# Performance work log

Hardware: AMD Instinct MI355X
Metric: run time of the kernel (lower is better)

## Reference

```python
import jax, jax.numpy as jnp
import numpy as np

N, P, C, H, W = 2, 100, 256, 128, 192
K = 3; KK = K * K; E = C * KK; NH = 8; DH = E // NH; FFN = 2048


def _ln(x, g, b, eps=1e-5):
    m = x.mean(-1, keepdims=True)
    v = ((x - m) ** 2).mean(-1, keepdims=True)
    return (x - m) * jax.lax.rsqrt(v + eps) * g + b


def setup_inputs():
    ks = iter(jax.random.split(jax.random.key(0), 64))
    def rnd(shape, s=1.0):
        return jax.random.normal(next(ks), shape, jnp.float32) * s
    z = lambda *s: jnp.zeros(s, jnp.float32)
    o = lambda *s: jnp.ones(s, jnp.float32)
    return {
        'x': rnd((N, C, H, W)),
        'proposal_feat': rnd((N, P, E)),
        'mask_preds': rnd((N, P, H, W)),
        'ku_dyn_w': rnd((2 * C, C), 0.02), 'ku_dyn_b': z(2 * C),
        'ku_in_w': rnd((2 * C, C), 0.02), 'ku_in_b': z(2 * C),
        'ku_ig_w': rnd((C, C), 0.02), 'ku_ig_b': z(C),
        'ku_ug_w': rnd((C, C), 0.02), 'ku_ug_b': z(C),
        'ku_nin_g': o(C), 'ku_nin_b': z(C),
        'ku_nout_g': o(C), 'ku_nout_b': z(C),
        'ku_inin_g': o(C), 'ku_inin_b': z(C),
        'ku_inout_g': o(C), 'ku_inout_b': z(C),
        'ku_fc_w': rnd((C, C), 0.02), 'ku_fc_b': z(C),
        'ku_fcn_g': o(C), 'ku_fcn_b': z(C),
        'attn_in_w': rnd((3 * E, E), 0.02), 'attn_in_b': z(3 * E),
        'attn_out_w': rnd((E, E), 0.02), 'attn_out_b': z(E),
        'attn_ln_g': o(E), 'attn_ln_b': z(E),
        'ffn_w1': rnd((FFN, C), 0.02), 'ffn_b1': z(FFN),
        'ffn_w2': rnd((C, FFN), 0.02), 'ffn_b2': z(C),
        'ffn_ln_g': o(C), 'ffn_ln_b': z(C),
        'mask_fc_ws': rnd((3, C, C), 0.02),
        'mask_fc_ln_g': o(3, C), 'mask_fc_ln_b': z(3, C),
        'fc_mask_w': rnd((C, C), 0.02), 'fc_mask_b': z(C),
    }


def _forward(x, proposal_feat, mask_preds, ku_dyn_w, ku_dyn_b, ku_in_w, ku_in_b,
             ku_ig_w, ku_ig_b, ku_ug_w, ku_ug_b, ku_nin_g, ku_nin_b, ku_nout_g,
             ku_nout_b, ku_inin_g, ku_inin_b, ku_inout_g, ku_inout_b, ku_fc_w,
             ku_fc_b, ku_fcn_g, ku_fcn_b, attn_in_w, attn_in_b, attn_out_w,
             attn_out_b, attn_ln_g, attn_ln_b, ffn_w1, ffn_b1, ffn_w2, ffn_b2,
             ffn_ln_g, ffn_ln_b, mask_fc_ws, mask_fc_ln_g, mask_fc_ln_b,
             fc_mask_w, fc_mask_b):
    # mask-softmax pooling over proposals: (N,P,H,W) x (N,C,H,W) -> (N,P,C)
    sig = jax.nn.softmax(mask_preds, axis=1)
    x_feat = jnp.einsum('bnhw,bchw->bnc', sig, x)

    # KernelUpdator (gated dynamic kernel update)
    pf = proposal_feat.reshape(N, P, C, KK).transpose(0, 1, 3, 2).reshape(N * P, KK, C)
    upd = x_feat.reshape(N * P, C)
    params = upd @ ku_dyn_w.T + ku_dyn_b            # (NP, 2C)
    p_in, p_out = params[:, :C], params[:, C:]
    inp = pf @ ku_in_w.T + ku_in_b                  # (NP, KK, 2C)
    i_in, i_out = inp[..., :C], inp[..., C:]
    gate = i_in * p_in[:, None, :]                  # (NP, KK, C)
    ig = jax.nn.sigmoid(_ln(gate @ ku_ig_w.T + ku_ig_b, ku_inin_g, ku_inin_b))
    ug = jax.nn.sigmoid(_ln(gate @ ku_ug_w.T + ku_ug_b, ku_nin_g, ku_nin_b))
    p_out = _ln(p_out, ku_nout_g, ku_nout_b)
    i_out = _ln(i_out, ku_inout_g, ku_inout_b)
    feat = ug * p_out[:, None, :] + ig * i_out
    feat = jax.nn.relu(_ln(feat @ ku_fc_w.T + ku_fc_b, ku_fcn_g, ku_fcn_b))  # (NP,KK,C)

    # self-attention across proposals; embed dim E = C*K*K, with residual + LN
    obj = feat.reshape(N, P, E).transpose(1, 0, 2)  # (P,N,E)
    qkv = obj @ attn_in_w.T + attn_in_b
    q, k, v = jnp.split(qkv, 3, axis=-1)
    q = q.reshape(P, N, NH, DH) * np.float32(1.0 / np.sqrt(DH))
    k = k.reshape(P, N, NH, DH)
    v = v.reshape(P, N, NH, DH)
    a = jax.nn.softmax(jnp.einsum('qnhd,knhd->nhqk', q, k), axis=-1)
    o = jnp.einsum('nhqk,knhd->qnhd', a, v).reshape(P, N, E)
    obj = _ln(obj + o @ attn_out_w.T + attn_out_b, attn_ln_g, attn_ln_b)
    obj = obj.transpose(1, 0, 2).reshape(N, P, KK, C)

    # FFN (residual) + LN, applied per (proposal, kernel position)
    h = jax.nn.relu(obj @ ffn_w1.T + ffn_b1) @ ffn_w2.T + ffn_b2
    obj = _ln(obj + h, ffn_ln_g, ffn_ln_b)

    mf = obj
    for i in range(3):
        mf = jax.nn.relu(_ln(mf @ mask_fc_ws[i].T, mask_fc_ln_g[i], mask_fc_ln_b[i]))
    mf = mf @ fc_mask_w.T + fc_mask_b               # (N,P,KK,C)
    kernels = mf.transpose(0, 1, 3, 2).reshape(N, P, C, K, K)

    # per-image dynamic conv: vmap replaces the python loop over batch
    def conv_one(xi, wi):
        return jax.lax.conv_general_dilated(
            xi[None], wi, (1, 1), 'SAME',
            dimension_numbers=('NCHW', 'OIHW', 'NCHW'))[0]
    new_masks = jax.vmap(conv_one)(x, kernels)      # (N,P,H,W)

    obj_kernels = obj.transpose(0, 1, 3, 2).reshape(N, P, C, K, K)
    return new_masks, obj_kernels


def reference(x, proposal_feat, mask_preds, ku_dyn_w, ku_dyn_b, ku_in_w, ku_in_b,
              ku_ig_w, ku_ig_b, ku_ug_w, ku_ug_b, ku_nin_g, ku_nin_b, ku_nout_g,
              ku_nout_b, ku_inin_g, ku_inin_b, ku_inout_g, ku_inout_b, ku_fc_w,
              ku_fc_b, ku_fcn_g, ku_fcn_b, attn_in_w, attn_in_b, attn_out_w,
              attn_out_b, attn_ln_g, attn_ln_b, ffn_w1, ffn_b1, ffn_w2, ffn_b2,
              ffn_ln_g, ffn_ln_b, mask_fc_ws, mask_fc_ln_g, mask_fc_ln_b,
              fc_mask_w, fc_mask_b):
    return _forward(x, proposal_feat, mask_preds, ku_dyn_w, ku_dyn_b, ku_in_w,
                    ku_in_b, ku_ig_w, ku_ig_b, ku_ug_w, ku_ug_b, ku_nin_g,
                    ku_nin_b, ku_nout_g, ku_nout_b, ku_inin_g, ku_inin_b,
                    ku_inout_g, ku_inout_b, ku_fc_w, ku_fc_b, ku_fcn_g, ku_fcn_b,
                    attn_in_w, attn_in_b, attn_out_w, attn_out_b, attn_ln_g,
                    attn_ln_b, ffn_w1, ffn_b1, ffn_w2, ffn_b2, ffn_ln_g,
                    ffn_ln_b, mask_fc_ws, mask_fc_ln_g, mask_fc_ln_b,
                    fc_mask_w, fc_mask_b)
```

## Files before the change

kernel.cpp:

```cpp
#include <hip/hip_runtime.h>
#include <hip/hip_bf16.h>

#define N_ 2
#define P_ 100
#define C_ 256
#define H_ 128
#define W_ 192
#define HW_ 24576
#define KK_ 9
#define E_ 2304
#define NH_ 8
#define DH_ 288
#define FFN_ 2048
#define NP_ 200
#define ROWS_ 1800
#define XKC_ 64

typedef __attribute__((ext_vector_type(8))) __bf16 bf16x8;
typedef __attribute__((ext_vector_type(4))) float f32x4;

__global__ __launch_bounds__(256) void k_softmax(const float* __restrict__ mp, float* __restrict__ sig){
  int idx = blockIdx.x*256 + threadIdx.x;
  if(idx >= N_*HW_) return;
  int n = idx / HW_, hw = idx - n*HW_;
  const float* base = mp + (size_t)n*P_*HW_ + hw;
  float m = -1e30f;
  for(int p=0;p<P_;p++) m = fmaxf(m, base[(size_t)p*HW_]);
  float s = 0.f;
  for(int p=0;p<P_;p++) s += __expf(base[(size_t)p*HW_] - m);
  float inv = 1.f/s;
  float* ob = sig + (size_t)n*P_*HW_ + hw;
  for(int p=0;p<P_;p++) ob[(size_t)p*HW_] = __expf(base[(size_t)p*HW_] - m)*inv;
}

__global__ __launch_bounds__(256) void k_permute_pf(const float* __restrict__ prop, float* __restrict__ pf){
  int i = blockIdx.x*256 + threadIdx.x;
  if(i >= ROWS_*C_) return;
  int c = i & 255;
  int r = i >> 8;
  int kk = r % 9, np = r / 9;
  pf[i] = prop[(size_t)np*E_ + c*KK_ + kk];
}

__global__ __launch_bounds__(256) void k_xfeat1m(const float* __restrict__ sig, const float* __restrict__ x,
                                                 float* __restrict__ partial){
  const int ct = blockIdx.x, kb = blockIdx.y, n = blockIdx.z;
  const int hw0 = kb*384;
  const int tid = threadIdx.x;
  const int wid = tid >> 6, lane = tid & 63;
  const int col = lane & 15, quad = lane >> 4;
  const int wm = wid & 1, wn = wid >> 1;
  const int MT = wm ? 3 : 4;
  __shared__ __bf16 As[112][72];
  __shared__ __bf16 Bs[128][72];
  f32x4 acc[4][4] = {};
  for(int k0=0; k0<384; k0+=64){
    __syncthreads();
    for(int i=tid; i<896; i+=256){
      int p = i >> 3, kg = i & 7;
      bf16x8 v;
      if(p < P_){
        const float* sp = &sig[((size_t)n*P_ + p)*HW_ + hw0 + k0 + kg*8];
        const float4 f0 = *(const float4*)sp;
        const float4 f1 = *(const float4*)(sp+4);
        v[0]=(__bf16)f0.x; v[1]=(__bf16)f0.y; v[2]=(__bf16)f0.z; v[3]=(__bf16)f0.w;
        v[4]=(__bf16)f1.x; v[5]=(__bf16)f1.y; v[6]=(__bf16)f1.z; v[7]=(__bf16)f1.w;
      } else {
        #pragma unroll
        for(int u=0;u<8;u++) v[u] = (__bf16)0.f;
      }
      *(bf16x8*)&As[p][kg*8] = v;
    }
    for(int i=tid; i<1024; i+=256){
      int c = i >> 3, kg = i & 7;
      const float* xp = &x[((size_t)n*C_ + ct*128 + c)*HW_ + hw0 + k0 + kg*8];
      const float4 f0 = *(const float4*)xp;
      const float4 f1 = *(const float4*)(xp+4);
      bf16x8 v;
      v[0]=(__bf16)f0.x; v[1]=(__bf16)f0.y; v[2]=(__bf16)f0.z; v[3]=(__bf16)f0.w;
      v[4]=(__bf16)f1.x; v[5]=(__bf16)f1.y; v[6]=(__bf16)f1.z; v[7]=(__bf16)f1.w;
      *(bf16x8*)&Bs[c][kg*8] = v;
    }
    __syncthreads();
    #pragma unroll
    for(int ks=0; ks<2; ks++){
      bf16x8 b[4];
      #pragma unroll
      for(int t=0;t<4;t++) b[t] = *(const bf16x8*)&Bs[(wn*4+t)*16 + col][ks*32 + quad*8];
      #pragma unroll
      for(int mt=0; mt<4; mt++){
        if(mt < MT){
          bf16x8 a = *(const bf16x8*)&As[(wm*4+mt)*16 + col][ks*32 + quad*8];
          #pragma unroll
          for(int t=0;t<4;t++)
            acc[mt][t] = __builtin_amdgcn_mfma_f32_16x16x32_bf16(a, b[t], acc[mt][t], 0, 0, 0);
        }
      }
    }
  }
  #pragma unroll
  for(int mt=0; mt<4; mt++){
    if(mt < MT){
      #pragma unroll
      for(int r=0;r<4;r++){
        int p = (wm*4+mt)*16 + quad*4 + r;
        if(p < P_){
          float* op = &partial[(((size_t)n*XKC_ + kb)*P_ + p)*C_ + ct*128 + wn*64 + col];
          #pragma unroll
          for(int t=0;t<4;t++) op[t*16] = acc[mt][t][r];
        }
      }
    }
  }
}

__global__ __launch_bounds__(256) void k_xfeat2(const float* __restrict__ partial, float* __restrict__ xfeat){
  int np = blockIdx.x;
  int n = np / P_, p = np - n*P_;
  int c = threadIdx.x;
  float s = 0.f;
  for(int kb=0;kb<XKC_;kb++) s += partial[(((size_t)n*XKC_ + kb)*P_ + p)*C_ + c];
  xfeat[(size_t)np*C_ + c] = s;
}

__global__ __launch_bounds__(256) void k_gemm_mfma(const float* __restrict__ A, const float* __restrict__ Wt,
    const float* __restrict__ bias, float* __restrict__ out, int M, int N, int K, int act)
{
  const int n0 = blockIdx.x*128, m0 = blockIdx.y*64;
  const int tid = threadIdx.x;
  const int wid = tid >> 6, lane = tid & 63;
  const int col = lane & 15, quad = lane >> 4;
  const int wm = wid & 1, wn = wid >> 1;
  __shared__ __bf16 As[64][72];
  __shared__ __bf16 Bs[128][72];
  f32x4 acc[2][4] = {};
  for(int k0=0; k0<K; k0+=64){
    __syncthreads();
    for(int i=tid; i<512; i+=256){
      int r = i >> 3, kg = i & 7;
      int m = m0 + r;
      bf16x8 v;
      if(m < M){
        const float* ap = &A[(size_t)m*K + k0 + kg*8];
        const float4 f0 = *(const float4*)ap;
        const float4 f1 = *(const float4*)(ap+4);
        v[0]=(__bf16)f0.x; v[1]=(__bf16)f0.y; v[2]=(__bf16)f0.z; v[3]=(__bf16)f0.w;
        v[4]=(__bf16)f1.x; v[5]=(__bf16)f1.y; v[6]=(__bf16)f1.z; v[7]=(__bf16)f1.w;
      } else {
        #pragma unroll
        for(int u=0;u<8;u++) v[u] = (__bf16)0.f;
      }
      *(bf16x8*)&As[r][kg*8] = v;
    }
    for(int i=tid; i<1024; i+=256){
      int r = i >> 3, kg = i & 7;
      const float* wp = &Wt[(size_t)(n0 + r)*K + k0 + kg*8];
      const float4 f0 = *(const float4*)wp;
      const float4 f1 = *(const float4*)(wp+4);
      bf16x8 v;
      v[0]=(__bf16)f0.x; v[1]=(__bf16)f0.y; v[2]=(__bf16)f0.z; v[3]=(__bf16)f0.w;
      v[4]=(__bf16)f1.x; v[5]=(__bf16)f1.y; v[6]=(__bf16)f1.z; v[7]=(__bf16)f1.w;
      *(bf16x8*)&Bs[r][kg*8] = v;
    }
    __syncthreads();
    #pragma unroll
    for(int ks=0; ks<2; ks++){
      bf16x8 b[4], a[2];
      #pragma unroll
      for(int t=0;t<4;t++) b[t] = *(const bf16x8*)&Bs[(wn*4+t)*16 + col][ks*32 + quad*8];
      #pragma unroll
      for(int mt=0;mt<2;mt++) a[mt] = *(const bf16x8*)&As[(wm*2+mt)*16 + col][ks*32 + quad*8];
      #pragma unroll
      for(int mt=0;mt<2;mt++)
        #pragma unroll
        for(int t=0;t<4;t++)
          acc[mt][t] = __builtin_amdgcn_mfma_f32_16x16x32_bf16(a[mt], b[t], acc[mt][t], 0, 0, 0);
    }
  }
  #pragma unroll
  for(int mt=0;mt<2;mt++){
    #pragma unroll
    for(int r=0;r<4;r++){
      int m = m0 + (wm*2+mt)*16 + quad*4 + r;
      if(m < M){
        #pragma unroll
        for(int t=0;t<4;t++){
          int n = n0 + (wn*4+t)*16 + col;
          float v = acc[mt][t][r];
          if(bias) v += bias[n];
          if(act == 1) v = fmaxf(v, 0.f);
          out[(size_t)m*N + n] = v;
        }
      }
    }
  }
}

__global__ __launch_bounds__(256) void k_gemm_splitk(const float* __restrict__ A, const float* __restrict__ Wt,
    float* __restrict__ part, int M, int N, int K, int KC)
{
  const int n0 = blockIdx.x*128, m0 = blockIdx.y*64;
  const int kz = blockIdx.z*KC;
  const int tid = threadIdx.x;
  const int wid = tid >> 6, lane = tid & 63;
  const int col = lane & 15, quad = lane >> 4;
  const int wm = wid & 1, wn = wid >> 1;
  __shared__ __bf16 As[64][72];
  __shared__ __bf16 Bs[128][72];
  f32x4 acc[2][4] = {};
  for(int k0=kz; k0<kz+KC; k0+=64){
    __syncthreads();
    for(int i=tid; i<512; i+=256){
      int r = i >> 3, kg = i & 7;
      int m = m0 + r;
      bf16x8 v;
      if(m < M){
        const float* ap = &A[(size_t)m*K + k0 + kg*8];
        const float4 f0 = *(const float4*)ap;
        const float4 f1 = *(const float4*)(ap+4);
        v[0]=(__bf16)f0.x; v[1]=(__bf16)f0.y; v[2]=(__bf16)f0.z; v[3]=(__bf16)f0.w;
        v[4]=(__bf16)f1.x; v[5]=(__bf16)f1.y; v[6]=(__bf16)f1.z; v[7]=(__bf16)f1.w;
      } else {
        #pragma unroll
        for(int u=0;u<8;u++) v[u] = (__bf16)0.f;
      }
      *(bf16x8*)&As[r][kg*8] = v;
    }
    for(int i=tid; i<1024; i+=256){
      int r = i >> 3, kg = i & 7;
      const float* wp = &Wt[(size_t)(n0 + r)*K + k0 + kg*8];
      const float4 f0 = *(const float4*)wp;
      const float4 f1 = *(const float4*)(wp+4);
      bf16x8 v;
      v[0]=(__bf16)f0.x; v[1]=(__bf16)f0.y; v[2]=(__bf16)f0.z; v[3]=(__bf16)f0.w;
      v[4]=(__bf16)f1.x; v[5]=(__bf16)f1.y; v[6]=(__bf16)f1.z; v[7]=(__bf16)f1.w;
      *(bf16x8*)&Bs[r][kg*8] = v;
    }
    __syncthreads();
    #pragma unroll
    for(int ks=0; ks<2; ks++){
      bf16x8 b[4], a[2];
      #pragma unroll
      for(int t=0;t<4;t++) b[t] = *(const bf16x8*)&Bs[(wn*4+t)*16 + col][ks*32 + quad*8];
      #pragma unroll
      for(int mt=0;mt<2;mt++) a[mt] = *(const bf16x8*)&As[(wm*2+mt)*16 + col][ks*32 + quad*8];
      #pragma unroll
      for(int mt=0;mt<2;mt++)
        #pragma unroll
        for(int t=0;t<4;t++)
          acc[mt][t] = __builtin_amdgcn_mfma_f32_16x16x32_bf16(a[mt], b[t], acc[mt][t], 0, 0, 0);
    }
  }
  float* pbase = part + (size_t)blockIdx.z*M*N;
  #pragma unroll
  for(int mt=0;mt<2;mt++){
    #pragma unroll
    for(int r=0;r<4;r++){
      int m = m0 + (wm*2+mt)*16 + quad*4 + r;
      if(m < M){
        #pragma unroll
        for(int t=0;t<4;t++){
          int n = n0 + (wn*4+t)*16 + col;
          pbase[(size_t)m*N + n] = acc[mt][t][r];
        }
      }
    }
  }
}

__global__ __launch_bounds__(256) void k_redk(const float* __restrict__ part, const float* __restrict__ bias,
    float* __restrict__ out, int M, int N, int S)
{
  size_t i4 = ((size_t)blockIdx.x*256 + threadIdx.x)*4;
  size_t MN = (size_t)M*N;
  if(i4 >= MN) return;
  float4 s = *(const float4*)&part[i4];
  for(int z=1; z<S; z++){
    const float4 p = *(const float4*)&part[(size_t)z*MN + i4];
    s.x+=p.x; s.y+=p.y; s.z+=p.z; s.w+=p.w;
  }
  if(bias){
    int n = (int)(i4 % (size_t)N);
    const float4 b = *(const float4*)&bias[n];
    s.x+=b.x; s.y+=b.y; s.z+=b.z; s.w+=b.w;
  }
  *(float4*)&out[i4] = s;
}

__global__ __launch_bounds__(256) void k_ln256(const float* __restrict__ in, const float* __restrict__ res,
    const float* __restrict__ g, const float* __restrict__ b, float* __restrict__ out, int M, int act)
{
  int row = blockIdx.x*4 + (threadIdx.x >> 6);
  int lane = threadIdx.x & 63;
  if(row >= M) return;
  float4 v = *(const float4*)&in[(size_t)row*C_ + lane*4];
  if(res){
    const float4 rv = *(const float4*)&res[(size_t)row*C_ + lane*4];
    v.x += rv.x; v.y += rv.y; v.z += rv.z; v.w += rv.w;
  }
  float s = v.x + v.y + v.z + v.w;
  float q = v.x*v.x + v.y*v.y + v.z*v.z + v.w*v.w;
  #pragma unroll
  for(int off=32; off; off>>=1){ s += __shfl_xor(s, off, 64); q += __shfl_xor(q, off, 64); }
  float mean = s*(1.f/256.f);
  float rstd = rsqrtf(q*(1.f/256.f) - mean*mean + 1e-5f);
  const float4 gv = *(const float4*)&g[lane*4];
  const float4 bv = *(const float4*)&b[lane*4];
  float o[4] = {(v.x-mean)*rstd*gv.x + bv.x, (v.y-mean)*rstd*gv.y + bv.y,
                (v.z-mean)*rstd*gv.z + bv.z, (v.w-mean)*rstd*gv.w + bv.w};
  #pragma unroll
  for(int j=0;j<4;j++){
    if(act==1) o[j] = fmaxf(o[j], 0.f);
    else if(act==2) o[j] = 1.f/(1.f + __expf(-o[j]));
  }
  float4 ov = {o[0],o[1],o[2],o[3]};
  *(float4*)&out[(size_t)row*C_ + lane*4] = ov;
}

__global__ __launch_bounds__(256) void k_gate(const float* __restrict__ inp, const float* __restrict__ params,
                                              float* __restrict__ gate){
  int i = blockIdx.x*256 + threadIdx.x;
  if(i >= ROWS_*C_) return;
  int c = i & 255, r = i >> 8;
  int np = r / 9;
  gate[i] = inp[(size_t)r*512 + c] * params[(size_t)np*512 + c];
}

__device__ __forceinline__ void block_stats(float v, float* red, int slot, float& mean, float& rstd){
  float s = v, q = v*v;
  #pragma unroll
  for(int off=32; off; off>>=1){ s += __shfl_xor(s, off, 64); q += __shfl_xor(q, off, 64); }
  int wid = threadIdx.x >> 6;
  if((threadIdx.x & 63) == 0){ red[slot + wid] = s; red[slot + 4 + wid] = q; }
  __syncthreads();
  s = red[slot+0]+red[slot+1]+red[slot+2]+red[slot+3];
  q = red[slot+4]+red[slot+5]+red[slot+6]+red[slot+7];
  mean = s*(1.f/256.f);
  rstd = rsqrtf(q*(1.f/256.f) - mean*mean + 1e-5f);
}

__global__ __launch_bounds__(256) void k_combine(const float* __restrict__ params, const float* __restrict__ inp,
  const float* __restrict__ ug, const float* __restrict__ ig,
  const float* __restrict__ nout_g, const float* __restrict__ nout_b,
  const float* __restrict__ inout_g, const float* __restrict__ inout_b,
  float* __restrict__ feat)
{
  __shared__ float red[16];
  int r = blockIdx.x;
  int np = r / 9;
  int c = threadIdx.x;
  float pv = params[(size_t)np*512 + 256 + c];
  float mean, rstd;
  block_stats(pv, red, 0, mean, rstd);
  float pn = (pv - mean)*rstd*nout_g[c] + nout_b[c];
  float iv = inp[(size_t)r*512 + 256 + c];
  float mean2, rstd2;
  block_stats(iv, red, 8, mean2, rstd2);
  float iw = (iv - mean2)*rstd2*inout_g[c] + inout_b[c];
  size_t o = (size_t)r*C_ + c;
  feat[o] = ug[o]*pn + ig[o]*iw;
}

__global__ __launch_bounds__(256) void k_attn2(const float* __restrict__ qkv, float* __restrict__ attnO){
  const int qt = blockIdx.x, h = blockIdx.y, n = blockIdx.z;
  const int q0 = qt*10;
  const int tid = threadIdx.x;
  __shared__ float Qs[10][292];
  __shared__ float KVs[25][292];
  __shared__ float Ss[10][104];
  const float scale = 0.05892556509887896f;
  const size_t base = (size_t)n*P_*6912 + (size_t)h*DH_;
  for(int i=tid; i<10*DH_; i+=256){
    int qi = i/DH_, d = i - qi*DH_;
    Qs[qi][d] = qkv[base + (size_t)(q0+qi)*6912 + d] * scale;
  }
  for(int kt=0; kt<4; kt++){
    int kp0 = kt*25;
    __syncthreads();
    for(int i=tid; i<25*DH_; i+=256){
      int ki = i/DH_, d = i - ki*DH_;
      KVs[ki][d] = qkv[base + (size_t)(kp0+ki)*6912 + E_ + d];
    }
    __syncthreads();
    if(tid < 250){
      int qi = tid/25, ki = tid - qi*25;
      float s = 0.f;
      #pragma unroll 9
      for(int d=0; d<DH_; d+=4){
        const float4 a = *(const float4*)&Qs[qi][d];
        const float4 b = *(const float4*)&KVs[ki][d];
        s += a.x*b.x + a.y*b.y + a.z*b.z + a.w*b.w;
      }
      Ss[qi][kp0+ki] = s;
    }
  }
  __syncthreads();
  {
    int w = tid >> 6, lane = tid & 63;
    for(int r=w; r<10; r+=4){
      float v0 = (lane < 100) ? Ss[r][lane] : -1e30f;
      float v1 = (lane < 36)  ? Ss[r][64+lane] : -1e30f;
      float m = fmaxf(v0, v1);
      #pragma unroll
      for(int off=32; off; off>>=1) m = fmaxf(m, __shfl_xor(m, off, 64));
      float e0 = (lane < 100) ? __expf(v0-m) : 0.f;
      float e1 = (lane < 36)  ? __expf(v1-m) : 0.f;
      float s = e0 + e1;
      #pragma unroll
      for(int off=32; off; off>>=1) s += __shfl_xor(s, off, 64);
      float inv = 1.f/s;
      if(lane < 100) Ss[r][lane] = e0*inv;
      if(lane < 36)  Ss[r][64+lane] = e1*inv;
    }
  }
  float acc[12];
  #pragma unroll
  for(int j=0;j<12;j++) acc[j]=0.f;
  for(int kt=0; kt<4; kt++){
    int kp0 = kt*25;
    __syncthreads();
    for(int i=tid; i<25*DH_; i+=256){
      int ki = i/DH_, d = i - ki*DH_;
      KVs[ki][d] = qkv[base + (size_t)(kp0+ki)*6912 + 2*E_ + d];
    }
    __syncthreads();
    int j = 0;
    for(int i=tid; i<10*DH_; i+=256, j++){
      int qi = i/DH_, d = i - qi*DH_;
      float s = acc[j];
      #pragma unroll
      for(int ki=0; ki<25; ki++) s += Ss[qi][kp0+ki]*KVs[ki][d];
      acc[j] = s;
    }
  }
  {
    int j = 0;
    for(int i=tid; i<10*DH_; i+=256, j++){
      int qi = i/DH_, d = i - qi*DH_;
      attnO[(size_t)(n*P_ + q0 + qi)*E_ + h*DH_ + d] = acc[j];
    }
  }
}

__global__ __launch_bounds__(256) void k_add_ln2304(const float* __restrict__ obj0, const float* __restrict__ tp,
  const float* __restrict__ g, const float* __restrict__ b, float* __restrict__ out)
{
  __shared__ float red[8];
  int row = blockIdx.x;
  float v[9]; float s=0.f, q=0.f;
  #pragma unroll
  for(int j=0;j<9;j++){
    int e = threadIdx.x + j*256;
    float t = obj0[(size_t)row*E_ + e] + tp[(size_t)row*E_ + e];
    v[j]=t; s+=t; q+=t*t;
  }
  #pragma unroll
  for(int off=32; off; off>>=1){ s += __shfl_xor(s, off, 64); q += __shfl_xor(q, off, 64); }
  int wid = threadIdx.x>>6;
  if((threadIdx.x&63)==0){ red[wid]=s; red[4+wid]=q; }
  __syncthreads();
  s = red[0]+red[1]+red[2]+red[3]; q = red[4]+red[5]+red[6]+red[7];
  float mean = s*(1.f/2304.f);
  float rstd = rsqrtf(q*(1.f/2304.f) - mean*mean + 1e-5f);
  #pragma unroll
  for(int j=0;j<9;j++){
    int e = threadIdx.x + j*256;
    out[(size_t)row*E_ + e] = (v[j]-mean)*rstd*g[e] + b[e];
  }
}

__global__ __launch_bounds__(256) void k_objk(const float* __restrict__ obj2, float* __restrict__ outk){
  int i = blockIdx.x*256 + threadIdx.x;
  if(i >= ROWS_*C_) return;
  int kk = i % 9; int t = i / 9; int c = t & 255; int np = t >> 8;
  outk[i] = obj2[((size_t)np*9 + kk)*C_ + c];
}

__global__ __launch_bounds__(256) void k_conv_mfma(const float* __restrict__ x, const float* __restrict__ ker,
                                                   float* __restrict__ out){
  const int wt = blockIdx.x, ht = blockIdx.y, z = blockIdx.z;
  const int n = z >> 1, ps = z & 1;
  const int pbase = ps*64;
  const int NT = ps ? 3 : 4;
  const int tid = threadIdx.x;
  const int hi = tid >> 6;
  const int lane = tid & 63;
  const int col = lane & 15, quad = lane >> 4;
  const int w0 = wt*64, h0 = ht*4;

  __shared__ __bf16 xs[6][66][32];
  __shared__ __bf16 ks[9][64][32];

  f32x4 acc[4][4] = {};
  const int npr = NT*16;

  for(int c0=0; c0<C_; c0+=32){
    __syncthreads();
    for(int i=tid; i<1584; i+=256){
      int oct = i / 396;
      int rem = i - oct*396;
      int hy = rem / 66, wx = rem - hy*66;
      int hh = h0 - 1 + hy, ww = w0 - 1 + wx;
      bf16x8 v;
      if(hh >= 0 && hh < H_ && ww >= 0 && ww < W_){
        const float* xp = &x[(((size_t)n*C_ + c0 + oct*8)*H_ + hh)*W_ + ww];
        #pragma unroll
        for(int u=0;u<8;u++) v[u] = (__bf16)xp[(size_t)u*HW_];
      } else {
        #pragma unroll
        for(int u=0;u<8;u++) v[u] = (__bf16)0.f;
      }
      *(bf16x8*)&xs[hy][wx][oct*8] = v;
    }
    for(int i=tid; i<9*npr*4; i+=256){
      int oct = i & 3;
      int t = i >> 2;
      int tap = t / npr, pl = t - tap*npr;
      int p = pbase + pl;
      bf16x8 v;
      if(p < P_){
        const float* kp = &ker[((size_t)(n*P_+p)*9 + tap)*C_ + c0 + oct*8];
        #pragma unroll
        for(int u=0;u<8;u++) v[u] = (__bf16)kp[u];
      } else {
        #pragma unroll
        for(int u=0;u<8;u++) v[u] = (__bf16)0.f;
      }
      *(bf16x8*)&ks[tap][pl][oct*8] = v;
    }
    __syncthreads();
    #pragma unroll
    for(int ky=0; ky<3; ky++){
      #pragma unroll
      for(int kx=0; kx<3; kx++){
        const int tap = ky*3 + kx;
        const int hy = hi + ky;
        bf16x8 b[4];
        #pragma unroll
        for(int t=0;t<4;t++) b[t] = *(const bf16x8*)&xs[hy][t*16 + col + kx][quad*8];
        #pragma unroll
        for(int pt=0; pt<4; pt++){
          if(pt < NT){
            bf16x8 a = *(const bf16x8*)&ks[tap][pt*16 + col][quad*8];
            #pragma unroll
            for(int t=0;t<4;t++)
              acc[pt][t] = __builtin_amdgcn_mfma_f32_16x16x32_bf16(a, b[t], acc[pt][t], 0, 0, 0);
          }
        }
      }
    }
  }
  const int h = h0 + hi;
  #pragma unroll
  for(int pt=0; pt<4; pt++){
    if(pt < NT){
      #pragma unroll
      for(int r=0;r<4;r++){
        int p = pbase + pt*16 + quad*4 + r;
        if(p < P_){
          float* op = &out[((size_t)(n*P_+p)*H_ + h)*W_ + w0 + col];
          #pragma unroll
          for(int t=0;t<4;t++) op[t*16] = acc[pt][t][r];
        }
      }
    }
  }
}

extern "C" void kernel_launch(void* const* d_in, const int* in_sizes, int n_in,
                              void* d_out, int out_size, void* d_ws, size_t ws_size,
                              hipStream_t stream)
{
  (void)in_sizes; (void)n_in; (void)out_size; (void)ws_size;
  const float* x          = (const float*)d_in[0];
  const float* prop       = (const float*)d_in[1];
  const float* mask_pred  = (const float*)d_in[2];
  const float* ku_dyn_w   = (const float*)d_in[3];
  const float* ku_dyn_b   = (const float*)d_in[4];
  const float* ku_in_w    = (const float*)d_in[5];
  const float* ku_in_b    = (const float*)d_in[6];
  const float* ku_ig_w    = (const float*)d_in[7];
  const float* ku_ig_b    = (const float*)d_in[8];
  const float* ku_ug_w    = (const float*)d_in[9];
  const float* ku_ug_b    = (const float*)d_in[10];
  const float* ku_nin_g   = (const float*)d_in[11];
  const float* ku_nin_b   = (const float*)d_in[12];
  const float* ku_nout_g  = (const float*)d_in[13];
  const float* ku_nout_b  = (const float*)d_in[14];
  const float* ku_inin_g  = (const float*)d_in[15];
  const float* ku_inin_b  = (const float*)d_in[16];
  const float* ku_inout_g = (const float*)d_in[17];
  const float* ku_inout_b = (const float*)d_in[18];
  const float* ku_fc_w    = (const float*)d_in[19];
  const float* ku_fc_b    = (const float*)d_in[20];
  const float* ku_fcn_g   = (const float*)d_in[21];
  const float* ku_fcn_b   = (const float*)d_in[22];
  const float* attn_in_w  = (const float*)d_in[23];
  const float* attn_in_b  = (const float*)d_in[24];
  const float* attn_out_w = (const float*)d_in[25];
  const float* attn_out_b = (const float*)d_in[26];
  const float* attn_ln_g  = (const float*)d_in[27];
  const float* attn_ln_b  = (const float*)d_in[28];
  const float* ffn_w1     = (const float*)d_in[29];
  const float* ffn_b1     = (const float*)d_in[30];
  const float* ffn_w2     = (const float*)d_in[31];
  const float* ffn_b2     = (const float*)d_in[32];
  const float* ffn_ln_g   = (const float*)d_in[33];
  const float* ffn_ln_b   = (const float*)d_in[34];
  const float* mask_fc_ws = (const float*)d_in[35];
  const float* mask_fc_ln_g = (const float*)d_in[36];
  const float* mask_fc_ln_b = (const float*)d_in[37];
  const float* fc_mask_w  = (const float*)d_in[38];
  const float* fc_mask_b  = (const float*)d_in[39];

  float* ws = (float*)d_ws;
  float* sig     = ws;
  float* hbuf    = ws;
  float* skA     = ws;
  float* partial = ws + 4915200;
  float* qkv     = ws + 4915200;
  float* skB     = ws + 4915200;
  float* attnO   = ws + 4915200 + 1382400;
  float* tproj   = ws + 4915200 + 1843200;
  float* tmp     = ws + 4915200 + 2304000;
  float* xfeat   = ws + 9830400;
  float* params  = xfeat + 51200;
  float* pf      = params + 102400;
  float* inp     = pf + 460800;
  float* gate    = inp + 921600;
  float* ig      = gate + 460800;
  float* ug      = ig + 460800;
  float* feat    = ug + 460800;
  float* obj0    = feat + 460800;
  float* obj1    = obj0 + 460800;
  float* obj2    = obj1 + 460800;
  float* mf1     = obj2 + 460800;
  float* mf2     = mf1 + 460800;
  float* mfF     = mf2 + 460800;

  float* out_masks = (float*)d_out;
  float* out_kern  = out_masks + (size_t)N_*P_*HW_;

  k_softmax<<<192, 256, 0, stream>>>(mask_pred, sig);
  k_permute_pf<<<1800, 256, 0, stream>>>(prop, pf);
  k_xfeat1m<<<dim3(2,XKC_,2), 256, 0, stream>>>(sig, x, partial);
  k_xfeat2<<<200, 256, 0, stream>>>(partial, xfeat);
  k_gemm_mfma<<<dim3(4,4),   256, 0, stream>>>(xfeat, ku_dyn_w, ku_dyn_b, params, 200, 512, 256, 0);
  k_gemm_mfma<<<dim3(4,29),  256, 0, stream>>>(pf, ku_in_w, ku_in_b, inp, 1800, 512, 256, 0);
  k_gate<<<1800, 256, 0, stream>>>(inp, params, gate);
  k_gemm_mfma<<<dim3(2,29),  256, 0, stream>>>(gate, ku_ig_w, ku_ig_b, tmp, 1800, 256, 256, 0);
  k_ln256<<<450, 256, 0, stream>>>(tmp, nullptr, ku_inin_g, ku_inin_b, ig, 1800, 2);
  k_gemm_mfma<<<dim3(2,29),  256, 0, stream>>>(gate, ku_ug_w, ku_ug_b, tmp, 1800, 256, 256, 0);
  k_ln256<<<450, 256, 0, stream>>>(tmp, nullptr, ku_nin_g, ku_nin_b, ug, 1800, 2);
  k_combine<<<1800, 256, 0, stream>>>(params, inp, ug, ig, ku_nout_g, ku_nout_b, ku_inout_g, ku_inout_b, feat);
  k_gemm_mfma<<<dim3(2,29),  256, 0, stream>>>(feat, ku_fc_w, ku_fc_b, tmp, 1800, 256, 256, 0);
  k_ln256<<<450, 256, 0, stream>>>(tmp, nullptr, ku_fcn_g, ku_fcn_b, obj0, 1800, 1);
  k_gemm_splitk<<<dim3(54,4,3), 256, 0, stream>>>(obj0, attn_in_w, skA, 200, 6912, 2304, 768);
  k_redk<<<1350, 256, 0, stream>>>(skA, attn_in_b, qkv, 200, 6912, 3);
  k_attn2<<<dim3(10,8,2), 256, 0, stream>>>(qkv, attnO);
  k_gemm_splitk<<<dim3(18,4,4), 256, 0, stream>>>(attnO, attn_out_w, skA, 200, 2304, 2304, 576);
  k_redk<<<450, 256, 0, stream>>>(skA, attn_out_b, tproj, 200, 2304, 4);
  k_add_ln2304<<<200, 256, 0, stream>>>(obj0, tproj, attn_ln_g, attn_ln_b, obj1);
  k_gemm_mfma<<<dim3(16,29), 256, 0, stream>>>(obj1, ffn_w1, ffn_b1, hbuf, 1800, 2048, 256, 1);
  k_gemm_splitk<<<dim3(2,29,4), 256, 0, stream>>>(hbuf, ffn_w2, skB, 1800, 256, 2048, 512);
  k_redk<<<450, 256, 0, stream>>>(skB, ffn_b2, tmp, 1800, 256, 4);
  k_ln256<<<450, 256, 0, stream>>>(tmp, obj1, ffn_ln_g, ffn_ln_b, obj2, 1800, 0);
  k_gemm_mfma<<<dim3(2,29),  256, 0, stream>>>(obj2, mask_fc_ws,          nullptr, tmp, 1800, 256, 256, 0);
  k_ln256<<<450, 256, 0, stream>>>(tmp, nullptr, mask_fc_ln_g,       mask_fc_ln_b,       mf1, 1800, 1);
  k_gemm_mfma<<<dim3(2,29),  256, 0, stream>>>(mf1,  mask_fc_ws + 65536,  nullptr, tmp, 1800, 256, 256, 0);
  k_ln256<<<450, 256, 0, stream>>>(tmp, nullptr, mask_fc_ln_g + 256, mask_fc_ln_b + 256, mf2, 1800, 1);
  k_gemm_mfma<<<dim3(2,29),  256, 0, stream>>>(mf2,  mask_fc_ws + 131072, nullptr, tmp, 1800, 256, 256, 0);
  k_ln256<<<450, 256, 0, stream>>>(tmp, nullptr, mask_fc_ln_g + 512, mask_fc_ln_b + 512, mf1, 1800, 1);
  k_gemm_mfma<<<dim3(2,29),  256, 0, stream>>>(mf1, fc_mask_w, fc_mask_b, mfF, 1800, 256, 256, 0);
  k_objk<<<1800, 256, 0, stream>>>(obj2, out_kern);
  k_conv_mfma<<<dim3(3,32,4), 256, 0, stream>>>(x, mfF, out_masks);
}
```

Before: 728.0 us.

## Pre-convert conv input to channel-octet bf16 layout and emit bf16 kernels

Adds a prep kernel that transposes x into a bf16 layout with 8 channels packed per spatial position. The conv can then load each 16-byte octet with one vector read instead of eight strided fp32 gathers that are re-read for every proposal tile. The final mask-FC GEMM now writes bf16 directly so the kernel-weight loads are vectorised too, and both shared-memory tiles are reorganised to [oct][pos][8] to reduce bank conflicts. This costs one extra pass over x and a workspace buffer aliased at the start of ws, which must not overlap any buffer still live at that point.

```diff
diff --git a/kernel.cpp b/kernel.cpp
--- a/kernel.cpp
+++ b/kernel.cpp
@@ -189,7 +189,8 @@
           float v = acc[mt][t][r];
           if(bias) v += bias[n];
           if(act == 1) v = fmaxf(v, 0.f);
-          out[(size_t)m*N + n] = v;
+          if(act == 3) ((__bf16*)out)[(size_t)m*N + n] = (__bf16)v;
+          else out[(size_t)m*N + n] = v;
         }
       }
     }
@@ -476,7 +477,20 @@
   outk[i] = obj2[((size_t)np*9 + kk)*C_ + c];
 }
 
-__global__ __launch_bounds__(256) void k_conv_mfma(const float* __restrict__ x, const float* __restrict__ ker,
+__global__ __launch_bounds__(256) void k_prep_x(const float* __restrict__ x, __bf16* __restrict__ xT){
+  int i = blockIdx.x*256 + threadIdx.x;
+  if(i >= N_*32*H_*W_) return;
+  int w = i % W_; int t = i / W_;
+  int h = t % H_; t /= H_;
+  int g = t % 32; int n = t / 32;
+  const float* xp = &x[((size_t)(n*C_ + g*8)*H_ + h)*W_ + w];
+  bf16x8 v;
+  #pragma unroll
+  for(int u=0;u<8;u++) v[u] = (__bf16)xp[(size_t)u*HW_];
+  *(bf16x8*)&xT[(size_t)i*8] = v;
+}
+
+__global__ __launch_bounds__(256) void k_conv_mfma(const __bf16* __restrict__ xT, const __bf16* __restrict__ kerb,
                                                    float* __restrict__ out){
   const int wt = blockIdx.x, ht = blockIdx.y, z = blockIdx.z;
   const int n = z >> 1, ps = z & 1;
@@ -488,11 +502,10 @@
   const int col = lane & 15, quad = lane >> 4;
   const int w0 = wt*64, h0 = ht*4;
 
-  __shared__ __bf16 xs[6][66][32];
-  __shared__ __bf16 ks[9][64][32];
+  __shared__ __bf16 xs[6][4][66][8];
+  __shared__ __bf16 ks[9][4][64][8];
 
   f32x4 acc[4][4] = {};
-  const int npr = NT*16;
 
   for(int c0=0; c0<C_; c0+=32){
     __syncthreads();
@@ -503,30 +516,26 @@
       int hh = h0 - 1 + hy, ww = w0 - 1 + wx;
       bf16x8 v;
       if(hh >= 0 && hh < H_ && ww >= 0 && ww < W_){
-        const float* xp = &x[(((size_t)n*C_ + c0 + oct*8)*H_ + hh)*W_ + ww];
-        #pragma unroll
-        for(int u=0;u<8;u++) v[u] = (__bf16)xp[(size_t)u*HW_];
+        v = *(const bf16x8*)&xT[((((size_t)n*32 + (c0>>3) + oct)*H_ + hh)*W_ + ww)*8];
       } else {
         #pragma unroll
         for(int u=0;u<8;u++) v[u] = (__bf16)0.f;
       }
-      *(bf16x8*)&xs[hy][wx][oct*8] = v;
-    }
-    for(int i=tid; i<9*npr*4; i+=256){
-      int oct = i & 3;
-      int t = i >> 2;
-      int tap = t / npr, pl = t - tap*npr;
+      *(bf16x8*)&xs[hy][oct][wx][0] = v;
+    }
+    for(int i=tid; i<2304; i+=256){
+      int oct = i / 576;
+      int r2 = i - oct*576;
+      int tap = r2 >> 6, pl = r2 & 63;
       int p = pbase + pl;
       bf16x8 v;
       if(p < P_){
-        const float* kp = &ker[((size_t)(n*P_+p)*9 + tap)*C_ + c0 + oct*8];
-        #pragma unroll
-        for(int u=0;u<8;u++) v[u] = (__bf16)kp[u];
+        v = *(const bf16x8*)&kerb[((size_t)(n*P_+p)*9 + tap)*C_ + c0 + oct*8];
       } else {
         #pragma unroll
         for(int u=0;u<8;u++) v[u] = (__bf16)0.f;
       }
-      *(bf16x8*)&ks[tap][pl][oct*8] = v;
+      *(bf16x8*)&ks[tap][oct][pl][0] = v;
     }
     __syncthreads();
     #pragma unroll
@@ -537,11 +546,11 @@
         const int hy = hi + ky;
         bf16x8 b[4];
         #pragma unroll
-        for(int t=0;t<4;t++) b[t] = *(const bf16x8*)&xs[hy][t*16 + col + kx][quad*8];
+        for(int t=0;t<4;t++) b[t] = *(const bf16x8*)&xs[hy][quad][t*16 + col + kx][0];
         #pragma unroll
         for(int pt=0; pt<4; pt++){
           if(pt < NT){
-            bf16x8 a = *(const bf16x8*)&ks[tap][pt*16 + col][quad*8];
+            bf16x8 a = *(const bf16x8*)&ks[tap][quad][pt*16 + col][0];
             #pragma unroll
             for(int t=0;t<4;t++)
               acc[pt][t] = __builtin_amdgcn_mfma_f32_16x16x32_bf16(a, b[t], acc[pt][t], 0, 0, 0);
@@ -637,6 +646,7 @@
   float* mf1     = obj2 + 460800;
   float* mf2     = mf1 + 460800;
   float* mfF     = mf2 + 460800;
+  __bf16* xT = (__bf16*)ws;
 
   float* out_masks = (float*)d_out;
   float* out_kern  = out_masks + (size_t)N_*P_*HW_;
@@ -671,7 +681,8 @@
   k_ln256<<<450, 256, 0, stream>>>(tmp, nullptr, mask_fc_ln_g + 256, mask_fc_ln_b + 256, mf2, 1800, 1);
   k_gemm_mfma<<<dim3(2,29),  256, 0, stream>>>(mf2,  mask_fc_ws + 131072, nullptr, tmp, 1800, 256, 256, 0);
   k_ln256<<<450, 256, 0, stream>>>(tmp, nullptr, mask_fc_ln_g + 512, mask_fc_ln_b + 512, mf1, 1800, 1);
-  k_gemm_mfma<<<dim3(2,29),  256, 0, stream>>>(mf1, fc_mask_w, fc_mask_b, mfF, 1800, 256, 256, 0);
+  k_gemm_mfma<<<dim3(2,29),  256, 0, stream>>>(mf1, fc_mask_w, fc_mask_b, mfF, 1800, 256, 256, 3);
   k_objk<<<1800, 256, 0, stream>>>(obj2, out_kern);
-  k_conv_mfma<<<dim3(3,32,4), 256, 0, stream>>>(x, mfF, out_masks);
-}
+  k_prep_x<<<6144, 256, 0, stream>>>(x, xT);
+  k_conv_mfma<<<dim3(3,32,4), 256, 0, stream>>>(xT, (const __bf16*)mfF, out_masks);
+}
```

Measured after the change: 739.4 us. About the same (+1.6%).
